# Kernel tuning notes

Hardware: AMD Instinct MI355X
Metric: run time of the kernel (lower is better)

The kernel has to match this reference:

```python
import jax, jax.numpy as jnp
import numpy as np

EPS = 1e-5  # torch InstanceNorm1d default eps
H = 64      # band_features


def instance_norm(x):
    # x: [B, T, F]; torch applies InstanceNorm1d on [B, F, T], i.e. normalize
    # over the length axis T per (batch, channel). No affine params.
    mu = jnp.mean(x, axis=1, keepdims=True)
    var = jnp.var(x, axis=1, keepdims=True)  # biased variance, as torch
    return (x - mu) * jax.lax.rsqrt(var + EPS)


def lstm_layer(x, Wih, Whh, bih, bhh):
    # x: [B, T, D_in]; Wih: [4H, D_in]; Whh: [4H, H]; gate order i,f,g,o (torch)
    B, T, _ = x.shape
    xp = jnp.einsum('btd,gd->btg', x, Wih) + bih + bhh   # [B, T, 4H]
    xp = jnp.swapaxes(xp, 0, 1)                          # [T, B, 4H]

    def step(carry, xt):
        h, c = carry
        gates = xt + h @ Whh.T                           # [B, 4H]
        i, f, g, o = jnp.split(gates, 4, axis=-1)
        c = jax.nn.sigmoid(f) * c + jax.nn.sigmoid(i) * jnp.tanh(g)
        h = jax.nn.sigmoid(o) * jnp.tanh(c)
        return (h, c), h

    h0 = jnp.zeros((B, H), x.dtype)
    _, hs = jax.lax.scan(step, (h0, h0), xp)             # hs: [T, B, H]
    return jnp.swapaxes(hs, 0, 1)                        # [B, T, H]


def setup_inputs() -> dict:
    key = jax.random.key(0)
    ks = jax.random.split(key, 12)
    B, T = 64, 4096
    bound = 1.0 / np.sqrt(H)  # torch LSTM/Linear default init scale

    def u(k, shape):
        return jax.random.uniform(k, shape, jnp.float32, -bound, bound)

    return {
        'x': jax.random.normal(ks[0], (B, T, H), jnp.float32),
        'Wih0': u(ks[1], (4 * H, H)), 'Whh0': u(ks[2], (4 * H, H)),
        'bih0': u(ks[3], (4 * H,)),   'bhh0': u(ks[4], (4 * H,)),
        'Wih1': u(ks[5], (4 * H, H)), 'Whh1': u(ks[6], (4 * H, H)),
        'bih1': u(ks[7], (4 * H,)),   'bhh1': u(ks[8], (4 * H,)),
        'Wfc': u(ks[9], (H, H)),      'bfc': u(ks[10], (H,)),
    }


def reference(x, Wih0, Whh0, bih0, bhh0, Wih1, Whh1, bih1, bhh1, Wfc, bfc):
    out = instance_norm(x)
    out = lstm_layer(out, Wih0, Whh0, bih0, bhh0)
    out = lstm_layer(out, Wih1, Whh1, bih1, bhh1)
    out = jnp.einsum('bth,oh->bto', out, Wfc) + bfc
    return out + x
```

## Files before the change

kernel.cpp:

```cpp
#include <hip/hip_runtime.h>
#include <cstddef>
#include <cstdint>

#define BB 64
#define TT 4096
#define HD 64
#define FP 72

typedef _Float16 f16;
typedef _Float16 f16x8 __attribute__((ext_vector_type(8)));
typedef _Float16 f16x4 __attribute__((ext_vector_type(4)));
typedef _Float16 f16x2 __attribute__((ext_vector_type(2)));
typedef float f32x4 __attribute__((ext_vector_type(4)));
typedef float v2f __attribute__((ext_vector_type(2)));

__device__ __forceinline__ void bar_lgkm() {
    asm volatile("s_waitcnt lgkmcnt(0)\n\ts_barrier" ::: "memory");
}

__global__ __launch_bounds__(256) void stats_part(const float* __restrict__ x,
                                                  float* __restrict__ part) {
    const int b = blockIdx.x >> 2, seg = blockIdx.x & 3;
    const int f = threadIdx.x & 63, grp = threadIdx.x >> 6;
    const float* xb = x + (size_t)b * TT * HD + (size_t)seg * (TT / 4) * HD;
    float s = 0.f, s2 = 0.f;
    for (int t = grp; t < TT / 4; t += 4) {
        float v = xb[t * HD + f];
        s += v;
        s2 = fmaf(v, v, s2);
    }
    __shared__ float ls[4][64];
    __shared__ float ls2[4][64];
    ls[grp][f] = s;
    ls2[grp][f] = s2;
    __syncthreads();
    if (threadIdx.x < 64) {
        float ss = 0.f, ss2 = 0.f;
#pragma unroll
        for (int i = 0; i < 4; ++i) { ss += ls[i][f]; ss2 += ls2[i][f]; }
        part[blockIdx.x * HD + f] = ss;
        part[256 * HD + blockIdx.x * HD + f] = ss2;
    }
}

__global__ __launch_bounds__(64) void stats_fin(const float* __restrict__ part,
                                                float* __restrict__ stats) {
    const int b = blockIdx.x, f = threadIdx.x;
    float s = 0.f, s2 = 0.f;
#pragma unroll
    for (int seg = 0; seg < 4; ++seg) {
        s += part[(b * 4 + seg) * HD + f];
        s2 += part[256 * HD + (b * 4 + seg) * HD + f];
    }
    float mu = s * (1.0f / TT);
    float var = s2 * (1.0f / TT) - mu * mu;
    stats[b * HD + f] = mu;
    stats[BB * HD + b * HD + f] = rsqrtf(var + 1e-5f);
}

__global__ __launch_bounds__(512, 2) void rnn_mfma(
    const float* __restrict__ x,
    const float* __restrict__ Wih0, const float* __restrict__ Whh0,
    const float* __restrict__ bih0, const float* __restrict__ bhh0,
    const float* __restrict__ Wih1, const float* __restrict__ Whh1,
    const float* __restrict__ bih1, const float* __restrict__ bhh1,
    const float* __restrict__ stats,
    float* __restrict__ h1out) {
    const int blk = blockIdx.x;
    const int tid = threadIdx.x;
    const int lane = tid & 63;
    const int wid = tid >> 6;
    const bool L1w = (wid < 4);
    const int wq = wid & 3;
    const int ln15 = lane & 15;
    const int l16 = lane >> 4;

    __shared__ __align__(16) f16 hT0[2][16 * FP];
    __shared__ __align__(16) f16 hT1[16][16 * FP];
    __shared__ __align__(16) f16 xnb[2][8][16 * FP];

    const float* WA = L1w ? Wih1 : Whh0;
    const float* WBm = L1w ? Whh1 : Wih0;
    uint32_t aA[4][2][4], aB[4][2][4];
#pragma unroll
    for (int i = 0; i < 4; ++i) {
        const int row = 64 * i + 16 * wq + ln15;
        const float sc = (i == 2) ? 2.88539008f : -1.44269504f;
#pragma unroll
        for (int kt = 0; kt < 2; ++kt) {
            const int fb = 32 * kt + 8 * l16;
            const float4 a0 = *(const float4*)&WA[row * HD + fb];
            const float4 a1 = *(const float4*)&WA[row * HD + fb + 4];
            const float4 b0 = *(const float4*)&WBm[row * HD + fb];
            const float4 b1 = *(const float4*)&WBm[row * HD + fb + 4];
            f16x8 ha = {(f16)(a0.x * sc), (f16)(a0.y * sc), (f16)(a0.z * sc), (f16)(a0.w * sc),
                        (f16)(a1.x * sc), (f16)(a1.y * sc), (f16)(a1.z * sc), (f16)(a1.w * sc)};
            f16x8 hb = {(f16)(b0.x * sc), (f16)(b0.y * sc), (f16)(b0.z * sc), (f16)(b0.w * sc),
                        (f16)(b1.x * sc), (f16)(b1.y * sc), (f16)(b1.z * sc), (f16)(b1.w * sc)};
            uint4 ua = __builtin_bit_cast(uint4, ha);
            uint4 ub = __builtin_bit_cast(uint4, hb);
            asm volatile("v_accvgpr_write_b32 %0, %1" : "=a"(aA[i][kt][0]) : "v"(ua.x));
            asm volatile("v_accvgpr_write_b32 %0, %1" : "=a"(aA[i][kt][1]) : "v"(ua.y));
            asm volatile("v_accvgpr_write_b32 %0, %1" : "=a"(aA[i][kt][2]) : "v"(ua.z));
            asm volatile("v_accvgpr_write_b32 %0, %1" : "=a"(aA[i][kt][3]) : "v"(ua.w));
            asm volatile("v_accvgpr_write_b32 %0, %1" : "=a"(aB[i][kt][0]) : "v"(ub.x));
            asm volatile("v_accvgpr_write_b32 %0, %1" : "=a"(aB[i][kt][1]) : "v"(ub.y));
            asm volatile("v_accvgpr_write_b32 %0, %1" : "=a"(aB[i][kt][2]) : "v"(ub.z));
            asm volatile("v_accvgpr_write_b32 %0, %1" : "=a"(aB[i][kt][3]) : "v"(ub.w));
        }
    }
    f16x8 wAf[4][2], wBf[4][2];
#pragma unroll
    for (int i = 0; i < 4; ++i)
#pragma unroll
        for (int kt = 0; kt < 2; ++kt) {
            uint4 ua = {aA[i][kt][0], aA[i][kt][1], aA[i][kt][2], aA[i][kt][3]};
            uint4 ub = {aB[i][kt][0], aB[i][kt][1], aB[i][kt][2], aB[i][kt][3]};
            wAf[i][kt] = __builtin_bit_cast(f16x8, ua);
            wBf[i][kt] = __builtin_bit_cast(f16x8, ub);
        }

    const float* bi = L1w ? bih1 : bih0;
    const float* bh = L1w ? bhh1 : bhh0;
    f32x4 bias[4];
#pragma unroll
    for (int i = 0; i < 4; ++i) {
        const float sc = (i == 2) ? 2.88539008f : -1.44269504f;
#pragma unroll
        for (int r = 0; r < 4; ++r) {
            const int row = 64 * i + 16 * wq + 4 * l16 + r;
            bias[i][r] = (bi[row] + bh[row]) * sc;
        }
    }

    const int sb = tid >> 5;
    const int f2 = (tid & 31) * 2;
    const size_t gb = (size_t)blk * 16 + sb;
    const float mux = stats[gb * HD + f2];
    const float muy = stats[gb * HD + f2 + 1];
    const float rsx = stats[(size_t)BB * HD + gb * HD + f2];
    const float rsy = stats[(size_t)BB * HD + gb * HD + f2 + 1];
    const v2f aa = {rsx, rsy};
    const v2f bbv = {-mux * rsx, -muy * rsy};
    const float* xrow = x + gb * TT * HD;
    float* orow = h1out + gb * TT * HD;

    for (int i = tid; i < 2 * 16 * FP / 2; i += 512) ((unsigned*)hT0)[i] = 0u;
    for (int i = tid; i < 16 * 16 * FP / 2; i += 512) ((unsigned*)hT1)[i] = 0u;

    v2f xr[8];
#pragma unroll
    for (int tau = 0; tau < 8; ++tau) {
        v2f v = *(const v2f*)&xrow[(size_t)tau * HD + f2];
        f16x2 xh;
        xh.x = (f16)fmaf(v.x, aa.x, bbv.x);
        xh.y = (f16)fmaf(v.y, aa.y, bbv.y);
        *(f16x2*)&xnb[0][tau][sb * FP + f2] = xh;
    }
#pragma unroll
    for (int tau = 0; tau < 8; ++tau)
        xr[tau] = *(const v2f*)&xrow[(size_t)(8 + tau) * HD + f2];

    v2f cstp[2] = {{0.f, 0.f}, {0.f, 0.f}};

    auto PHASE = [&](const f16* src1, const f16* src2, f16* dest) {
        f16x8 B1k0 = *(const f16x8*)&src1[ln15 * FP + 8 * l16];
        f16x8 B1k1 = *(const f16x8*)&src1[ln15 * FP + 32 + 8 * l16];
        f16x8 B2k0 = *(const f16x8*)&src2[ln15 * FP + 8 * l16];
        f16x8 B2k1 = *(const f16x8*)&src2[ln15 * FP + 32 + 8 * l16];
        f32x4 acc[4];
#pragma unroll
        for (int i = 0; i < 4; ++i) {
            acc[i] = bias[i];
            acc[i] = __builtin_amdgcn_mfma_f32_16x16x32_f16(wAf[i][0], B1k0, acc[i], 0, 0, 0);
            acc[i] = __builtin_amdgcn_mfma_f32_16x16x32_f16(wAf[i][1], B1k1, acc[i], 0, 0, 0);
            acc[i] = __builtin_amdgcn_mfma_f32_16x16x32_f16(wBf[i][0], B2k0, acc[i], 0, 0, 0);
            acc[i] = __builtin_amdgcn_mfma_f32_16x16x32_f16(wBf[i][1], B2k1, acc[i], 0, 0, 0);
        }
        uint32_t hw[2];
#pragma unroll
        for (int rp = 0; rp < 2; ++rp) {
            v2f gi = {acc[0][2 * rp], acc[0][2 * rp + 1]};
            v2f gf = {acc[1][2 * rp], acc[1][2 * rp + 1]};
            v2f gg = {acc[2][2 * rp], acc[2][2 * rp + 1]};
            v2f go = {acc[3][2 * rp], acc[3][2 * rp + 1]};
            v2f emi = {__builtin_amdgcn_exp2f(gi.x), __builtin_amdgcn_exp2f(gi.y)};
            v2f emf = {__builtin_amdgcn_exp2f(gf.x), __builtin_amdgcn_exp2f(gf.y)};
            v2f eg2 = {__builtin_amdgcn_exp2f(gg.x), __builtin_amdgcn_exp2f(gg.y)};
            v2f emo = {__builtin_amdgcn_exp2f(go.x), __builtin_amdgcn_exp2f(go.y)};
            v2f A = emi + 1.0f;
            v2f F = emf + 1.0f;
            v2f G2p = eg2 + 1.0f;
            v2f G2m = eg2 - 1.0f;
            v2f AG = A * G2p;
            v2f num = cstp[rp] * AG + G2m * F;
            v2f den = F * AG;
            v2f rc = {__builtin_amdgcn_rcpf(den.x), __builtin_amdgcn_rcpf(den.y)};
            v2f c = num * rc;
            cstp[rp] = c;
            v2f tc2 = c * 2.88539008f;
            v2f ec2 = {__builtin_amdgcn_exp2f(tc2.x), __builtin_amdgcn_exp2f(tc2.y)};
            v2f dno = (emo + 1.0f) * (ec2 + 1.0f);
            v2f rno = {__builtin_amdgcn_rcpf(dno.x), __builtin_amdgcn_rcpf(dno.y)};
            v2f h = (ec2 - 1.0f) * rno;
            f16x2 hh;
            hh.x = (f16)h.x;
            hh.y = (f16)h.y;
            hw[rp] = __builtin_bit_cast(uint32_t, hh);
        }
        uint2 hu = {hw[0], hw[1]};
        *(f16x4*)&dest[ln15 * FP + 16 * wq + 4 * l16] = __builtin_bit_cast(f16x4, hu);
    };

    bar_lgkm();
    if (!L1w) PHASE(&hT0[1][0], &xnb[0][0][0], &hT0[0][0]);
    bar_lgkm();

    for (int tb = 0; tb < TT; tb += 16) {
#pragma unroll
        for (int k = 0; k < 16; ++k) {
            {
                const f16* src1 = &hT0[k & 1][0];
                const f16* src2 = L1w ? &hT1[(k + 15) & 15][0]
                                      : &xnb[((k + 1) >> 3) & 1][(k + 1) & 7][0];
                f16* dest = L1w ? &hT1[k & 15][0] : &hT0[(k + 1) & 1][0];
                PHASE(src1, src2, dest);
            }
            if (tb > 0 || k >= 2) {
                f16x2 hh = *(const f16x2*)&hT1[(k + 14) & 15][sb * FP + f2];
                v2f o = {(float)hh.x, (float)hh.y};
                *(v2f*)&orow[(size_t)(tb + k - 2) * HD + f2] = o;
            }
            {
                const int tc = k & 7;
                if (k < 8 || tb < TT - 16) {
                    const int bufw = (k < 8) ? 1 : 0;
                    v2f v = xr[tc];
                    f16x2 xh;
                    xh.x = (f16)fmaf(v.x, aa.x, bbv.x);
                    xh.y = (f16)fmaf(v.y, aa.y, bbv.y);
                    *(f16x2*)&xnb[bufw][tc][sb * FP + f2] = xh;
                }
                if (tb < TT - 16) {
                    xr[tc] = *(const v2f*)&xrow[(size_t)(tb + 16 + k) * HD + f2];
                }
            }
            bar_lgkm();
        }
    }
    {
        f16x2 h14 = *(const f16x2*)&hT1[14][sb * FP + f2];
        v2f o14 = {(float)h14.x, (float)h14.y};
        *(v2f*)&orow[(size_t)(TT - 2) * HD + f2] = o14;
        f16x2 h15 = *(const f16x2*)&hT1[15][sb * FP + f2];
        v2f o15 = {(float)h15.x, (float)h15.y};
        *(v2f*)&orow[(size_t)(TT - 1) * HD + f2] = o15;
    }
}

__global__ __launch_bounds__(256) void fc_res(float* __restrict__ hout,
                                              const float* __restrict__ x,
                                              const float* __restrict__ Wfc,
                                              const float* __restrict__ bfc) {
    __shared__ __align__(16) float wfc_lds[HD * HD];
    __shared__ float bfc_lds[HD];
    const int tid = threadIdx.x;
#pragma unroll
    for (int i = 0; i < 4; ++i)
        ((float4*)wfc_lds)[tid + 256 * i] = ((const float4*)Wfc)[tid + 256 * i];
    if (tid < HD) bfc_lds[tid] = bfc[tid];

    const size_t row = (size_t)blockIdx.x * 256 + tid;
    float hr[HD];
    {
        const float4* hp = (const float4*)(hout + row * HD);
#pragma unroll
        for (int i = 0; i < 16; ++i) {
            float4 v = hp[i];
            hr[4 * i] = v.x; hr[4 * i + 1] = v.y;
            hr[4 * i + 2] = v.z; hr[4 * i + 3] = v.w;
        }
    }
    __syncthreads();

    const float4* xp = (const float4*)(x + row * HD);
    float4* op = (float4*)(hout + row * HD);
    for (int j4 = 0; j4 < 16; ++j4) {
        float s0 = 0.f, s1 = 0.f, s2 = 0.f, s3 = 0.f;
        const float* w0 = &wfc_lds[(4 * j4 + 0) * HD];
        const float* w1 = &wfc_lds[(4 * j4 + 1) * HD];
        const float* w2 = &wfc_lds[(4 * j4 + 2) * HD];
        const float* w3 = &wfc_lds[(4 * j4 + 3) * HD];
#pragma unroll
        for (int k = 0; k < HD; ++k) {
            s0 = fmaf(w0[k], hr[k], s0);
            s1 = fmaf(w1[k], hr[k], s1);
            s2 = fmaf(w2[k], hr[k], s2);
            s3 = fmaf(w3[k], hr[k], s3);
        }
        float4 xv = xp[j4];
        float4 o;
        o.x = s0 + bfc_lds[4 * j4 + 0] + xv.x;
        o.y = s1 + bfc_lds[4 * j4 + 1] + xv.y;
        o.z = s2 + bfc_lds[4 * j4 + 2] + xv.z;
        o.w = s3 + bfc_lds[4 * j4 + 3] + xv.w;
        op[j4] = o;
    }
}

extern "C" void kernel_launch(void* const* d_in, const int* in_sizes, int n_in,
                              void* d_out, int out_size, void* d_ws, size_t ws_size,
                              hipStream_t stream) {
    const float* x    = (const float*)d_in[0];
    const float* Wih0 = (const float*)d_in[1];
    const float* Whh0 = (const float*)d_in[2];
    const float* bih0 = (const float*)d_in[3];
    const float* bhh0 = (const float*)d_in[4];
    const float* Wih1 = (const float*)d_in[5];
    const float* Whh1 = (const float*)d_in[6];
    const float* bih1 = (const float*)d_in[7];
    const float* bhh1 = (const float*)d_in[8];
    const float* Wfc  = (const float*)d_in[9];
    const float* bfc  = (const float*)d_in[10];

    float* part  = (float*)d_ws;
    float* stats = part + 2 * 256 * HD;
    float* out   = (float*)d_out;

    stats_part<<<256, 256, 0, stream>>>(x, part);
    stats_fin<<<64, 64, 0, stream>>>(part, stats);
    rnn_mfma<<<4, 512, 0, stream>>>(x, Wih0, Whh0, bih0, bhh0,
                                    Wih1, Whh1, bih1, bhh1, stats, out);
    fc_res<<<1024, 256, 0, stream>>>(out, x, Wfc, bfc);
}
```

Measured before the change: 3.152 ms.

## Fuse FC projection and residual into recurrent kernel via MFMA per step

Removes the separate fc_res kernel. Each recurrent block now applies the final linear layer with fp16 MFMA on the layer-1 hidden state in LDS and writes the output directly. Even and odd steps alternate between the two wave groups. The residual is rebuilt from the fp16 normalized input already staged in LDS, which avoids rereading x and writing then rereading h. This trades a full-tensor memory pass and a launch for extra work inside the latency-bound recurrent loop, plus reduced residual precision.

```diff
diff --git a/kernel.cpp b/kernel.cpp
--- a/kernel.cpp
+++ b/kernel.cpp
@@ -64,8 +64,9 @@
     const float* __restrict__ bih0, const float* __restrict__ bhh0,
     const float* __restrict__ Wih1, const float* __restrict__ Whh1,
     const float* __restrict__ bih1, const float* __restrict__ bhh1,
+    const float* __restrict__ Wfc, const float* __restrict__ bfc,
     const float* __restrict__ stats,
-    float* __restrict__ h1out) {
+    float* __restrict__ outp) {
     const int blk = blockIdx.x;
     const int tid = threadIdx.x;
     const int lane = tid & 63;
@@ -120,6 +121,28 @@
             wBf[i][kt] = __builtin_bit_cast(f16x8, ub);
         }
 
+    uint32_t aF[2][4];
+#pragma unroll
+    for (int kt = 0; kt < 2; ++kt) {
+        const int rowF = 16 * wq + ln15;
+        const int fb = 32 * kt + 8 * l16;
+        const float4 c0 = *(const float4*)&Wfc[rowF * HD + fb];
+        const float4 c1 = *(const float4*)&Wfc[rowF * HD + fb + 4];
+        f16x8 hf = {(f16)c0.x, (f16)c0.y, (f16)c0.z, (f16)c0.w,
+                    (f16)c1.x, (f16)c1.y, (f16)c1.z, (f16)c1.w};
+        uint4 uf = __builtin_bit_cast(uint4, hf);
+        asm volatile("v_accvgpr_write_b32 %0, %1" : "=a"(aF[kt][0]) : "v"(uf.x));
+        asm volatile("v_accvgpr_write_b32 %0, %1" : "=a"(aF[kt][1]) : "v"(uf.y));
+        asm volatile("v_accvgpr_write_b32 %0, %1" : "=a"(aF[kt][2]) : "v"(uf.z));
+        asm volatile("v_accvgpr_write_b32 %0, %1" : "=a"(aF[kt][3]) : "v"(uf.w));
+    }
+    f16x8 wFcf[2];
+#pragma unroll
+    for (int kt = 0; kt < 2; ++kt) {
+        uint4 uf = {aF[kt][0], aF[kt][1], aF[kt][2], aF[kt][3]};
+        wFcf[kt] = __builtin_bit_cast(f16x8, uf);
+    }
+
     const float* bi = L1w ? bih1 : bih0;
     const float* bh = L1w ? bhh1 : bhh0;
     f32x4 bias[4];
@@ -132,6 +155,18 @@
             bias[i][r] = (bi[row] + bh[row]) * sc;
         }
     }
+
+    const int jF = 16 * wq + 4 * l16;
+    f32x4 bfcf;
+    {
+        const float4 bt = *(const float4*)&bfc[jF];
+        bfcf[0] = bt.x; bfcf[1] = bt.y; bfcf[2] = bt.z; bfcf[3] = bt.w;
+    }
+    const size_t gbF = (size_t)blk * 16 + ln15;
+    const float4 muF = *(const float4*)&stats[gbF * HD + jF];
+    const float4 rsF = *(const float4*)&stats[(size_t)BB * HD + gbF * HD + jF];
+    const float4 ivF = {1.0f / rsF.x, 1.0f / rsF.y, 1.0f / rsF.z, 1.0f / rsF.w};
+    float* oFC = outp + gbF * TT * HD + jF;
 
     const int sb = tid >> 5;
     const int f2 = (tid & 31) * 2;
@@ -143,7 +178,6 @@
     const v2f aa = {rsx, rsy};
     const v2f bbv = {-mux * rsx, -muy * rsy};
     const float* xrow = x + gb * TT * HD;
-    float* orow = h1out + gb * TT * HD;
 
     for (int i = tid; i < 2 * 16 * FP / 2; i += 512) ((unsigned*)hT0)[i] = 0u;
     for (int i = tid; i < 16 * 16 * FP / 2; i += 512) ((unsigned*)hT1)[i] = 0u;
@@ -212,6 +246,21 @@
         *(f16x4*)&dest[ln15 * FP + 16 * wq + 4 * l16] = __builtin_bit_cast(f16x4, hu);
     };
 
+    auto FCFLUSH = [&](const f16* hs, const f16* xs, float* optr) {
+        f16x8 Hk0 = *(const f16x8*)&hs[ln15 * FP + 8 * l16];
+        f16x8 Hk1 = *(const f16x8*)&hs[ln15 * FP + 32 + 8 * l16];
+        f32x4 o = bfcf;
+        o = __builtin_amdgcn_mfma_f32_16x16x32_f16(wFcf[0], Hk0, o, 0, 0, 0);
+        o = __builtin_amdgcn_mfma_f32_16x16x32_f16(wFcf[1], Hk1, o, 0, 0, 0);
+        f16x4 xnv = *(const f16x4*)&xs[ln15 * FP + jF];
+        float4 ov;
+        ov.x = o[0] + fmaf((float)xnv[0], ivF.x, muF.x);
+        ov.y = o[1] + fmaf((float)xnv[1], ivF.y, muF.y);
+        ov.z = o[2] + fmaf((float)xnv[2], ivF.z, muF.z);
+        ov.w = o[3] + fmaf((float)xnv[3], ivF.w, muF.w);
+        *(float4*)optr = ov;
+    };
+
     bar_lgkm();
     if (!L1w) PHASE(&hT0[1][0], &xnb[0][0][0], &hT0[0][0]);
     bar_lgkm();
@@ -227,9 +276,14 @@
                 PHASE(src1, src2, dest);
             }
             if (tb > 0 || k >= 2) {
-                f16x2 hh = *(const f16x2*)&hT1[(k + 14) & 15][sb * FP + f2];
-                v2f o = {(float)hh.x, (float)hh.y};
-                *(v2f*)&orow[(size_t)(tb + k - 2) * HD + f2] = o;
+                const bool mine = (k & 1) ? L1w : !L1w;
+                if (mine) {
+                    const int sh = (k + 14) & 15;
+                    const int px = (k >= 2 && k <= 9) ? 0 : 1;
+                    const int sx = (k + 6) & 7;
+                    FCFLUSH(&hT1[sh][0], &xnb[px][sx][0],
+                            oFC + (size_t)(tb + k - 2) * HD);
+                }
             }
             {
                 const int tc = k & 7;
@@ -248,64 +302,8 @@
             bar_lgkm();
         }
     }
-    {
-        f16x2 h14 = *(const f16x2*)&hT1[14][sb * FP + f2];
-        v2f o14 = {(float)h14.x, (float)h14.y};
-        *(v2f*)&orow[(size_t)(TT - 2) * HD + f2] = o14;
-        f16x2 h15 = *(const f16x2*)&hT1[15][sb * FP + f2];
-        v2f o15 = {(float)h15.x, (float)h15.y};
-        *(v2f*)&orow[(size_t)(TT - 1) * HD + f2] = o15;
-    }
-}
-
-__global__ __launch_bounds__(256) void fc_res(float* __restrict__ hout,
-                                              const float* __restrict__ x,
-                                              const float* __restrict__ Wfc,
-                                              const float* __restrict__ bfc) {
-    __shared__ __align__(16) float wfc_lds[HD * HD];
-    __shared__ float bfc_lds[HD];
-    const int tid = threadIdx.x;
-#pragma unroll
-    for (int i = 0; i < 4; ++i)
-        ((float4*)wfc_lds)[tid + 256 * i] = ((const float4*)Wfc)[tid + 256 * i];
-    if (tid < HD) bfc_lds[tid] = bfc[tid];
-
-    const size_t row = (size_t)blockIdx.x * 256 + tid;
-    float hr[HD];
-    {
-        const float4* hp = (const float4*)(hout + row * HD);
-#pragma unroll
-        for (int i = 0; i < 16; ++i) {
-            float4 v = hp[i];
-            hr[4 * i] = v.x; hr[4 * i + 1] = v.y;
-            hr[4 * i + 2] = v.z; hr[4 * i + 3] = v.w;
-        }
-    }
-    __syncthreads();
-
-    const float4* xp = (const float4*)(x + row * HD);
-    float4* op = (float4*)(hout + row * HD);
-    for (int j4 = 0; j4 < 16; ++j4) {
-        float s0 = 0.f, s1 = 0.f, s2 = 0.f, s3 = 0.f;
-        const float* w0 = &wfc_lds[(4 * j4 + 0) * HD];
-        const float* w1 = &wfc_lds[(4 * j4 + 1) * HD];
-        const float* w2 = &wfc_lds[(4 * j4 + 2) * HD];
-        const float* w3 = &wfc_lds[(4 * j4 + 3) * HD];
-#pragma unroll
-        for (int k = 0; k < HD; ++k) {
-            s0 = fmaf(w0[k], hr[k], s0);
-            s1 = fmaf(w1[k], hr[k], s1);
-            s2 = fmaf(w2[k], hr[k], s2);
-            s3 = fmaf(w3[k], hr[k], s3);
-        }
-        float4 xv = xp[j4];
-        float4 o;
-        o.x = s0 + bfc_lds[4 * j4 + 0] + xv.x;
-        o.y = s1 + bfc_lds[4 * j4 + 1] + xv.y;
-        o.z = s2 + bfc_lds[4 * j4 + 2] + xv.z;
-        o.w = s3 + bfc_lds[4 * j4 + 3] + xv.w;
-        op[j4] = o;
-    }
+    if (!L1w) FCFLUSH(&hT1[14][0], &xnb[1][6][0], oFC + (size_t)(TT - 2) * HD);
+    else      FCFLUSH(&hT1[15][0], &xnb[1][7][0], oFC + (size_t)(TT - 1) * HD);
 }
 
 extern "C" void kernel_launch(void* const* d_in, const int* in_sizes, int n_in,
@@ -330,6 +328,6 @@
     stats_part<<<256, 256, 0, stream>>>(x, part);
     stats_fin<<<64, 64, 0, stream>>>(part, stats);
     rnn_mfma<<<4, 512, 0, stream>>>(x, Wih0, Whh0, bih0, bhh0,
-                                    Wih1, Whh1, bih1, bhh1, stats, out);
-    fc_res<<<1024, 256, 0, stream>>>(out, x, Wfc, bfc);
-}
+                                    Wih1, Whh1, bih1, bhh1, Wfc, bfc,
+                                    stats, out);
+}
```

New measurement: 3.285 ms. +4.2%, slower.
